# Optimization experiments

Hardware: AMD Instinct MI355X
Metric: run time of the kernel (lower is better)

The kernel has to match this reference:

```python
import jax, jax.numpy as jnp
import numpy as np

V_TH = 1.0          # HeavisideBoxcar firing threshold
SUBTHRESH = 0.5     # boxcar surrogate half-width (affects backward only)
INIT_TAU = 2.0      # membrane time constant; decay = sigmoid(init_tau)

N_IN, N_HIDDEN = 784, 1024
BATCH, STEPS = 128, 500


def setup_inputs() -> dict:
    key = jax.random.key(0)
    kx, kf, kr = jax.random.split(key, 3)
    x = jax.random.uniform(kx, (BATCH, STEPS, N_IN), dtype=jnp.float32)
    fc1 = 0.05 * jax.random.uniform(kf, (N_IN, N_HIDDEN), dtype=jnp.float32) / np.sqrt(N_IN)
    recurrent = 0.05 * jax.random.uniform(kr, (N_HIDDEN, N_HIDDEN), dtype=jnp.float32) / np.sqrt(N_HIDDEN)
    return {"x": x, "fc1": fc1, "recurrent": recurrent}


def reference(x, fc1, recurrent):
    # x: [B, T, n_in]; leaky-integrate-and-fire recurrent scan over T.
    B, T, _ = x.shape
    n_hidden = fc1.shape[1]
    n_slice = n_hidden // 10
    decay = jax.nn.sigmoid(jnp.asarray(INIT_TAU, dtype=x.dtype))

    def step(carry, x_t):
        mem, spk = carry                                   # [B, H] each
        cur = x_t @ fc1 + spk @ recurrent                  # input + recurrent current
        mem = mem * decay * (1.0 - spk) + cur              # leaky integrate with reset-by-spike
        spk = (mem >= V_TH).astype(mem.dtype)              # heaviside fire
        return (mem, spk), spk[:, :n_slice]

    init = (jnp.zeros((B, n_hidden), x.dtype), jnp.zeros((B, n_hidden), x.dtype))
    _, outs = jax.lax.scan(step, init, jnp.swapaxes(x, 0, 1))   # outs: [T, B, n_slice]
    return jnp.swapaxes(outs, 0, 1), T
```

## Files before the change

kernel.cpp:

```cpp
#include <hip/hip_runtime.h>
#include <stdint.h>

#define T_STEPS 500
#define NBATCH  128
#define NIN     784
#define KPAD    832
#define NH      1024
#define NSL     102
#define DECAY   0.8807970779778823f

typedef __attribute__((ext_vector_type(8))) short short8;
typedef __attribute__((ext_vector_type(4))) float f32x4;
typedef unsigned int u32;
typedef unsigned long long u64;

static __device__ __forceinline__ unsigned short f2bf(float f) {
  union { float f; u32 u; } v; v.f = f;
  u32 r = (v.u + 0x7FFFu + ((v.u >> 16) & 1u)) >> 16;
  return (unsigned short)r;
}
static __device__ __forceinline__ float uf(u32 u) {
  union { u32 u; float f; } v; v.u = u; return v.f;
}
static __device__ __forceinline__ u32 fu(float f) {
  union { float f; u32 u; } v; v.f = f; return v.u;
}
static __device__ __forceinline__ void gl16(const void* g, void* l) {
  __builtin_amdgcn_global_load_lds((const __attribute__((address_space(1))) u32*)g,
                                   (__attribute__((address_space(3))) u32*)l, 16, 0, 0);
}

__global__ __launch_bounds__(256) void prep_kernel(
    const float* __restrict__ fc1, unsigned short* __restrict__ fc1T,
    float* __restrict__ out_last) {
  __shared__ float tile[32][33];
  const int bx = blockIdx.x;
  const int kb = (bx % 26) * 32, nb = (bx / 26) * 32;
  const int tx = threadIdx.x & 31, ty = threadIdx.x >> 5;
#pragma unroll
  for (int i = 0; i < 4; ++i) {
    int k = kb + ty + i * 8, n = nb + tx;
    tile[ty + i * 8][tx] = (k < NIN) ? fc1[(size_t)k * NH + n] : 0.0f;
  }
  __syncthreads();
#pragma unroll
  for (int i = 0; i < 4; ++i) {
    int n = nb + ty + i * 8, k = kb + tx;
    fc1T[(size_t)n * KPAD + k] = f2bf(tile[tx][ty + i * 8]);
  }
  if (bx == 0 && threadIdx.x == 0) *out_last = 500.0f;
}

__global__ __launch_bounds__(256, 2) void gemm_kernel(
    const float* __restrict__ x, const unsigned short* __restrict__ fc1T,
    const float* __restrict__ wrec, float* __restrict__ colsum,
    unsigned short* __restrict__ curq) {
  if (blockIdx.y == 500) {
    const int h = blockIdx.x * 256 + threadIdx.x;
    float s0 = 0.f, s1 = 0.f, s2 = 0.f, s3 = 0.f,
          s4 = 0.f, s5 = 0.f, s6 = 0.f, s7 = 0.f;
    for (int j = 0; j < NH; j += 8) {
      s0 += wrec[(size_t)(j + 0) * NH + h];
      s1 += wrec[(size_t)(j + 1) * NH + h];
      s2 += wrec[(size_t)(j + 2) * NH + h];
      s3 += wrec[(size_t)(j + 3) * NH + h];
      s4 += wrec[(size_t)(j + 4) * NH + h];
      s5 += wrec[(size_t)(j + 5) * NH + h];
      s6 += wrec[(size_t)(j + 6) * NH + h];
      s7 += wrec[(size_t)(j + 7) * NH + h];
    }
    colsum[h] = ((s0 + s1) + (s2 + s3)) + ((s4 + s5) + (s6 + s7));
    return;
  }

  __shared__ __align__(16) float Af[128 * 64];
  __shared__ __align__(16) unsigned short Bs[256 * 64];

  const int tid = threadIdx.x;
  const int n0 = blockIdx.x * 256, m0 = blockIdx.y * 128;
  const int lane = tid & 63, wave = tid >> 6;
  const int wr = (wave >> 1) * 64, wc = (wave & 1) * 128;
  const int l16 = lane & 15, q = lane >> 4;

  const int a_r = lane >> 4;
  const int a_pc = lane & 15;
  const int b_r = lane >> 3;
  const int b_pc = lane & 7;

  f32x4 acc[4][8];
  const f32x4 z4 = {0.f, 0.f, 0.f, 0.f};
#pragma unroll
  for (int i = 0; i < 4; ++i)
#pragma unroll
    for (int j = 0; j < 8; ++j) acc[i][j] = z4;

  for (int k0 = 0; k0 < KPAD; k0 += 64) {
#pragma unroll
    for (int l = 0; l < 8; ++l) {
      const int rbase = wave * 32 + l * 4;
      const int row = rbase + a_r;
      const int g = a_pc ^ (row & 15);
      if (k0 + g * 4 < NIN)
        gl16(x + (size_t)(m0 + row) * NIN + k0 + g * 4, &Af[rbase * 64]);
    }
#pragma unroll
    for (int l = 0; l < 8; ++l) {
      const int rbase = wave * 64 + l * 8;
      const int row = rbase + b_r;
      const int g = b_pc ^ (row & 7);
      gl16(fc1T + (size_t)(n0 + row) * KPAD + k0 + g * 8, &Bs[rbase * 64]);
    }
    __syncthreads();

#pragma unroll
    for (int h = 0; h < 2; ++h) {
      short8 av[4], bv[8];
#pragma unroll
      for (int i = 0; i < 4; ++i) {
        const int r = wr + i * 16 + l16;
        const int g0 = h * 8 + q * 2;
        const float4 alo = *(const float4*)&Af[r * 64 + ((g0)     ^ (r & 15)) * 4];
        const float4 ahi = *(const float4*)&Af[r * 64 + ((g0 + 1) ^ (r & 15)) * 4];
        union { short8 s; u32 u[4]; } p;
        p.u[0] = __builtin_amdgcn_perm(fu(alo.y), fu(alo.x), 0x07060302u);
        p.u[1] = __builtin_amdgcn_perm(fu(alo.w), fu(alo.z), 0x07060302u);
        p.u[2] = __builtin_amdgcn_perm(fu(ahi.y), fu(ahi.x), 0x07060302u);
        p.u[3] = __builtin_amdgcn_perm(fu(ahi.w), fu(ahi.z), 0x07060302u);
        av[i] = p.s;
      }
#pragma unroll
      for (int j = 0; j < 8; ++j) {
        const int r = wc + j * 16 + l16;
        const int c = h * 4 + q;
        bv[j] = *(const short8*)&Bs[r * 64 + ((c ^ (r & 7))) * 8];
      }
#pragma unroll
      for (int i = 0; i < 4; ++i)
#pragma unroll
        for (int j = 0; j < 8; ++j)
          acc[i][j] = __builtin_amdgcn_mfma_f32_16x16x32_bf16(av[i], bv[j],
                                                              acc[i][j], 0, 0, 0);
    }
    __syncthreads();
  }

#pragma unroll
  for (int i = 0; i < 4; ++i)
#pragma unroll
    for (int j = 0; j < 8; ++j) {
      const int row = m0 + wr + i * 16 + q * 4;
      const int col = n0 + wc + j * 16 + l16;
#pragma unroll
      for (int rr = 0; rr < 4; ++rr)
        curq[(size_t)(row + rr) * NH + col] = f2bf(acc[i][j][rr]);
    }
}

template <int NP, int NL>
static __device__ __forceinline__ void scan_blk(
    const int tb, const size_t rowbase, const int h0, const unsigned lane,
    const unsigned short* __restrict__ curq, const float* __restrict__ wrec,
    const float* __restrict__ colsum, float* __restrict__ out,
    uint4 (&cur)[8][2], uint4 (&nxt)[8][2],
    float (&mem)[16], float (&rs)[16], float (&sp)[16],
    u32& spbits, u32& chgpack, u64& pend) {
#pragma unroll
  for (int u = 0; u < NL; ++u) {
    const uint4* p = (const uint4*)&curq[(rowbase + tb + 8 + u) * NH + h0];
    nxt[u][0] = p[0];
    nxt[u][1] = p[1];
  }
#pragma unroll
  for (int u = 0; u < NP; ++u) {
    const int t = tb + u;

    if (__builtin_expect(pend != 0ull, 0)) {
      if (__popcll(pend) >= 48) {
#pragma unroll
        for (int c = 0; c < 16; c += 4) {
          const float4 cs = *(const float4*)&colsum[h0 + c];
          rs[c] = cs.x; rs[c + 1] = cs.y; rs[c + 2] = cs.z; rs[c + 3] = cs.w;
        }
        const u32 myz = (~spbits) & 0xFFFFu;
        u64 zm = __ballot(myz != 0);
        while (zm) {
          const int l = __builtin_ctzll(zm); zm &= zm - 1;
          u32 zb = __shfl(myz, l, 64);
          while (zb) {
            const int c = __builtin_ctz(zb); zb &= zb - 1;
            const float* w = &wrec[(size_t)(l * 16 + c) * NH + h0];
#pragma unroll
            for (int qq = 0; qq < 4; ++qq) {
              const float4 wv = *(const float4*)(w + 4 * qq);
              rs[4 * qq] -= wv.x; rs[4 * qq + 1] -= wv.y;
              rs[4 * qq + 2] -= wv.z; rs[4 * qq + 3] -= wv.w;
            }
          }
        }
      } else {
        u64 dm = pend;
        while (dm) {
          const int l = __builtin_ctzll(dm); dm &= dm - 1;
          const u32 pk = __shfl(chgpack, l, 64);
          u32 cbits = pk >> 16;
          while (cbits) {
            const int c = __builtin_ctz(cbits); cbits &= cbits - 1;
            const float s = ((pk >> c) & 1u) ? 1.0f : -1.0f;
            const float* w = &wrec[(size_t)(l * 16 + c) * NH + h0];
#pragma unroll
            for (int qq = 0; qq < 4; ++qq) {
              const float4 wv = *(const float4*)(w + 4 * qq);
              rs[4 * qq]     = fmaf(s, wv.x, rs[4 * qq]);
              rs[4 * qq + 1] = fmaf(s, wv.y, rs[4 * qq + 1]);
              rs[4 * qq + 2] = fmaf(s, wv.z, rs[4 * qq + 2]);
              rs[4 * qq + 3] = fmaf(s, wv.w, rs[4 * qq + 3]);
            }
          }
        }
      }
      pend = 0;
    }

    const uint4 Aa = cur[u][0], Bb = cur[u][1];
    const u32 dw[8] = {Aa.x, Aa.y, Aa.z, Aa.w, Bb.x, Bb.y, Bb.z, Bb.w};
    float cin[16];
#pragma unroll
    for (int k = 0; k < 8; ++k) {
      cin[2 * k]     = uf(dw[k] << 16);
      cin[2 * k + 1] = uf(dw[k] & 0xFFFF0000u);
    }

    u32 newbits = 0;
    float ns[16];
#pragma unroll
    for (int c = 0; c < 16; ++c) {
      const float f = fmaf(-DECAY, sp[c], DECAY);
      mem[c] = fmaf(mem[c], f, cin[c] + rs[c]);
      const bool fire = mem[c] >= 1.0f;
      ns[c] = fire ? 1.0f : 0.0f;
      newbits |= fire ? (1u << c) : 0u;
    }

    if (lane < 7) {
      float2* o = (float2*)(out + (rowbase + t) * NSL + h0);
      const int n2 = (lane == 6) ? 3 : 8;
#pragma unroll
      for (int k = 0; k < 8; ++k)
        if (k < n2) o[k] = make_float2(ns[2 * k], ns[2 * k + 1]);
    }

    const u32 chg = spbits ^ newbits;
    pend = __ballot(chg != 0);
    chgpack = (chg << 16) | newbits;
    spbits = newbits;
#pragma unroll
    for (int c = 0; c < 16; ++c) sp[c] = ns[c];
  }
}

__global__ __launch_bounds__(64, 1) void scan_kernel(
    const unsigned short* __restrict__ curq, const float* __restrict__ wrec,
    const float* __restrict__ colsum, float* __restrict__ out) {
  const int b = blockIdx.x;
  const unsigned lane = threadIdx.x;
  const int h0 = (int)lane * 16;
  const size_t rowbase = (size_t)b * T_STEPS;

  float mem[16], rs[16], sp[16];
#pragma unroll
  for (int c = 0; c < 16; ++c) { mem[c] = 0.f; rs[c] = 0.f; sp[c] = 0.f; }
  u32 spbits = 0, chgpack = 0;
  u64 pend = 0;

  uint4 A[8][2], B[8][2];
#pragma unroll
  for (int u = 0; u < 8; ++u) {
    const uint4* p = (const uint4*)&curq[(rowbase + u) * NH + h0];
    A[u][0] = p[0];
    A[u][1] = p[1];
  }

  int tb = 0;
#pragma unroll 1
  for (int it = 0; it < 30; ++it) {
    scan_blk<8, 8>(tb, rowbase, h0, lane, curq, wrec, colsum, out,
                   A, B, mem, rs, sp, spbits, chgpack, pend);
    scan_blk<8, 8>(tb + 8, rowbase, h0, lane, curq, wrec, colsum, out,
                   B, A, mem, rs, sp, spbits, chgpack, pend);
    tb += 16;
  }
  scan_blk<8, 8>(480, rowbase, h0, lane, curq, wrec, colsum, out,
                 A, B, mem, rs, sp, spbits, chgpack, pend);
  scan_blk<8, 4>(488, rowbase, h0, lane, curq, wrec, colsum, out,
                 B, A, mem, rs, sp, spbits, chgpack, pend);
  scan_blk<4, 0>(496, rowbase, h0, lane, curq, wrec, colsum, out,
                 A, B, mem, rs, sp, spbits, chgpack, pend);
}

extern "C" void kernel_launch(void* const* d_in, const int* in_sizes, int n_in,
                              void* d_out, int out_size, void* d_ws, size_t ws_size,
                              hipStream_t stream) {
  const float* x    = (const float*)d_in[0];
  const float* fc1  = (const float*)d_in[1];
  const float* wrec = (const float*)d_in[2];
  float* out = (float*)d_out;

  unsigned short* fc1T = (unsigned short*)d_ws;
  float* colsum = (float*)((char*)d_ws + 1703936);
  unsigned short* curq = (unsigned short*)((char*)d_ws + 1708032);

  prep_kernel<<<dim3(26 * 32), 256, 0, stream>>>(fc1, fc1T, out + (out_size - 1));
  gemm_kernel<<<dim3(4, 501), 256, 0, stream>>>(x, fc1T, wrec, colsum, curq);
  scan_kernel<<<dim3(NBATCH), 64, 0, stream>>>(curq, wrec, colsum, out);
}
```

Before: 632.2 us.

## Shrink GEMM tile, convert A to bf16 at load, and restructure scan prefetch

The GEMM tile changes from 128x256 to 128x128, doubling the grid and raising launch bounds to 3 blocks per SM. The fp32 x tile is now converted to bf16 in registers before it is written to LDS, which halves A's shared-memory footprint, and the extra colsum blocks are told to exit early. The scan kernel replaces the 8-deep double-buffered block prefetch with a 4-deep rolling per-row prefetch written as macros. These changes aim for higher occupancy and lower LDS use in the GEMM and less register pressure in the scan. The cost is a shallower prefetch distance in the serial scan, and the A loads become synchronous register loads instead of direct-to-LDS loads.

```diff
diff --git a/kernel.cpp b/kernel.cpp
--- a/kernel.cpp
+++ b/kernel.cpp
@@ -51,11 +51,12 @@
   if (bx == 0 && threadIdx.x == 0) *out_last = 500.0f;
 }
 
-__global__ __launch_bounds__(256, 2) void gemm_kernel(
+__global__ __launch_bounds__(256, 3) void gemm_kernel(
     const float* __restrict__ x, const unsigned short* __restrict__ fc1T,
     const float* __restrict__ wrec, float* __restrict__ colsum,
     unsigned short* __restrict__ curq) {
   if (blockIdx.y == 500) {
+    if (blockIdx.x >= 4) return;
     const int h = blockIdx.x * 256 + threadIdx.x;
     float s0 = 0.f, s1 = 0.f, s2 = 0.f, s3 = 0.f,
           s4 = 0.f, s5 = 0.f, s6 = 0.f, s7 = 0.f;
@@ -73,71 +74,76 @@
     return;
   }
 
-  __shared__ __align__(16) float Af[128 * 64];
-  __shared__ __align__(16) unsigned short Bs[256 * 64];
+  __shared__ __align__(16) unsigned short Aq[128 * 64];
+  __shared__ __align__(16) unsigned short Bs[128 * 64];
 
   const int tid = threadIdx.x;
-  const int n0 = blockIdx.x * 256, m0 = blockIdx.y * 128;
+  const int n0 = blockIdx.x * 128, m0 = blockIdx.y * 128;
   const int lane = tid & 63, wave = tid >> 6;
-  const int wr = (wave >> 1) * 64, wc = (wave & 1) * 128;
+  const int wr = (wave >> 1) * 64, wc = (wave & 1) * 64;
   const int l16 = lane & 15, q = lane >> 4;
 
-  const int a_r = lane >> 4;
-  const int a_pc = lane & 15;
-  const int b_r = lane >> 3;
-  const int b_pc = lane & 7;
-
-  f32x4 acc[4][8];
+  const int ar = tid >> 3;
+  const int ac = tid & 7;
+
+  f32x4 acc[4][4];
   const f32x4 z4 = {0.f, 0.f, 0.f, 0.f};
 #pragma unroll
   for (int i = 0; i < 4; ++i)
 #pragma unroll
-    for (int j = 0; j < 8; ++j) acc[i][j] = z4;
+    for (int j = 0; j < 4; ++j) acc[i][j] = z4;
 
   for (int k0 = 0; k0 < KPAD; k0 += 64) {
-#pragma unroll
-    for (int l = 0; l < 8; ++l) {
-      const int rbase = wave * 32 + l * 4;
-      const int row = rbase + a_r;
-      const int g = a_pc ^ (row & 15);
-      if (k0 + g * 4 < NIN)
-        gl16(x + (size_t)(m0 + row) * NIN + k0 + g * 4, &Af[rbase * 64]);
-    }
-#pragma unroll
-    for (int l = 0; l < 8; ++l) {
-      const int rbase = wave * 64 + l * 8;
-      const int row = rbase + b_r;
-      const int g = b_pc ^ (row & 7);
+    float4 fa[4][2];
+    const bool aval = (k0 + ac * 8) < NIN;
+#pragma unroll
+    for (int i = 0; i < 4; ++i) {
+      if (aval) {
+        const float4* src =
+            (const float4*)(x + (size_t)(m0 + i * 32 + ar) * NIN + k0 + ac * 8);
+        fa[i][0] = src[0];
+        fa[i][1] = src[1];
+      } else {
+        fa[i][0] = make_float4(0.f, 0.f, 0.f, 0.f);
+        fa[i][1] = make_float4(0.f, 0.f, 0.f, 0.f);
+      }
+    }
+#pragma unroll
+    for (int l = 0; l < 4; ++l) {
+      const int rbase = wave * 32 + l * 8;
+      const int row = rbase + (lane >> 3);
+      const int g = (lane & 7) ^ (row & 7);
       gl16(fc1T + (size_t)(n0 + row) * KPAD + k0 + g * 8, &Bs[rbase * 64]);
     }
+#pragma unroll
+    for (int i = 0; i < 4; ++i) {
+      union { short8 s; u32 u[4]; } p;
+      p.u[0] = __builtin_amdgcn_perm(fu(fa[i][0].y), fu(fa[i][0].x), 0x07060302u);
+      p.u[1] = __builtin_amdgcn_perm(fu(fa[i][0].w), fu(fa[i][0].z), 0x07060302u);
+      p.u[2] = __builtin_amdgcn_perm(fu(fa[i][1].y), fu(fa[i][1].x), 0x07060302u);
+      p.u[3] = __builtin_amdgcn_perm(fu(fa[i][1].w), fu(fa[i][1].z), 0x07060302u);
+      const int row = i * 32 + ar;
+      *(short8*)&Aq[row * 64 + (ac ^ (row & 7)) * 8] = p.s;
+    }
     __syncthreads();
 
 #pragma unroll
     for (int h = 0; h < 2; ++h) {
-      short8 av[4], bv[8];
+      short8 av[4], bv[4];
 #pragma unroll
       for (int i = 0; i < 4; ++i) {
         const int r = wr + i * 16 + l16;
-        const int g0 = h * 8 + q * 2;
-        const float4 alo = *(const float4*)&Af[r * 64 + ((g0)     ^ (r & 15)) * 4];
-        const float4 ahi = *(const float4*)&Af[r * 64 + ((g0 + 1) ^ (r & 15)) * 4];
-        union { short8 s; u32 u[4]; } p;
-        p.u[0] = __builtin_amdgcn_perm(fu(alo.y), fu(alo.x), 0x07060302u);
-        p.u[1] = __builtin_amdgcn_perm(fu(alo.w), fu(alo.z), 0x07060302u);
-        p.u[2] = __builtin_amdgcn_perm(fu(ahi.y), fu(ahi.x), 0x07060302u);
-        p.u[3] = __builtin_amdgcn_perm(fu(ahi.w), fu(ahi.z), 0x07060302u);
-        av[i] = p.s;
+        av[i] = *(const short8*)&Aq[r * 64 + ((h * 4 + q) ^ (r & 7)) * 8];
       }
 #pragma unroll
-      for (int j = 0; j < 8; ++j) {
+      for (int j = 0; j < 4; ++j) {
         const int r = wc + j * 16 + l16;
-        const int c = h * 4 + q;
-        bv[j] = *(const short8*)&Bs[r * 64 + ((c ^ (r & 7))) * 8];
+        bv[j] = *(const short8*)&Bs[r * 64 + ((h * 4 + q) ^ (r & 7)) * 8];
       }
 #pragma unroll
       for (int i = 0; i < 4; ++i)
 #pragma unroll
-        for (int j = 0; j < 8; ++j)
+        for (int j = 0; j < 4; ++j)
           acc[i][j] = __builtin_amdgcn_mfma_f32_16x16x32_bf16(av[i], bv[j],
                                                               acc[i][j], 0, 0, 0);
     }
@@ -147,7 +153,7 @@
 #pragma unroll
   for (int i = 0; i < 4; ++i)
 #pragma unroll
-    for (int j = 0; j < 8; ++j) {
+    for (int j = 0; j < 4; ++j) {
       const int row = m0 + wr + i * 16 + q * 4;
       const int col = n0 + wc + j * 16 + l16;
 #pragma unroll
@@ -156,107 +162,86 @@
     }
 }
 
-template <int NP, int NL>
-static __device__ __forceinline__ void scan_blk(
-    const int tb, const size_t rowbase, const int h0, const unsigned lane,
-    const unsigned short* __restrict__ curq, const float* __restrict__ wrec,
-    const float* __restrict__ colsum, float* __restrict__ out,
-    uint4 (&cur)[8][2], uint4 (&nxt)[8][2],
-    float (&mem)[16], float (&rs)[16], float (&sp)[16],
-    u32& spbits, u32& chgpack, u64& pend) {
-#pragma unroll
-  for (int u = 0; u < NL; ++u) {
-    const uint4* p = (const uint4*)&curq[(rowbase + tb + 8 + u) * NH + h0];
-    nxt[u][0] = p[0];
-    nxt[u][1] = p[1];
-  }
-#pragma unroll
-  for (int u = 0; u < NP; ++u) {
-    const int t = tb + u;
-
-    if (__builtin_expect(pend != 0ull, 0)) {
-      if (__popcll(pend) >= 48) {
-#pragma unroll
-        for (int c = 0; c < 16; c += 4) {
-          const float4 cs = *(const float4*)&colsum[h0 + c];
-          rs[c] = cs.x; rs[c + 1] = cs.y; rs[c + 2] = cs.z; rs[c + 3] = cs.w;
-        }
-        const u32 myz = (~spbits) & 0xFFFFu;
-        u64 zm = __ballot(myz != 0);
-        while (zm) {
-          const int l = __builtin_ctzll(zm); zm &= zm - 1;
-          u32 zb = __shfl(myz, l, 64);
-          while (zb) {
-            const int c = __builtin_ctz(zb); zb &= zb - 1;
-            const float* w = &wrec[(size_t)(l * 16 + c) * NH + h0];
-#pragma unroll
-            for (int qq = 0; qq < 4; ++qq) {
-              const float4 wv = *(const float4*)(w + 4 * qq);
-              rs[4 * qq] -= wv.x; rs[4 * qq + 1] -= wv.y;
-              rs[4 * qq + 2] -= wv.z; rs[4 * qq + 3] -= wv.w;
-            }
-          }
-        }
-      } else {
-        u64 dm = pend;
-        while (dm) {
-          const int l = __builtin_ctzll(dm); dm &= dm - 1;
-          const u32 pk = __shfl(chgpack, l, 64);
-          u32 cbits = pk >> 16;
-          while (cbits) {
-            const int c = __builtin_ctz(cbits); cbits &= cbits - 1;
-            const float s = ((pk >> c) & 1u) ? 1.0f : -1.0f;
-            const float* w = &wrec[(size_t)(l * 16 + c) * NH + h0];
-#pragma unroll
-            for (int qq = 0; qq < 4; ++qq) {
-              const float4 wv = *(const float4*)(w + 4 * qq);
-              rs[4 * qq]     = fmaf(s, wv.x, rs[4 * qq]);
-              rs[4 * qq + 1] = fmaf(s, wv.y, rs[4 * qq + 1]);
-              rs[4 * qq + 2] = fmaf(s, wv.z, rs[4 * qq + 2]);
-              rs[4 * qq + 3] = fmaf(s, wv.w, rs[4 * qq + 3]);
-            }
-          }
-        }
-      }
-      pend = 0;
-    }
-
-    const uint4 Aa = cur[u][0], Bb = cur[u][1];
-    const u32 dw[8] = {Aa.x, Aa.y, Aa.z, Aa.w, Bb.x, Bb.y, Bb.z, Bb.w};
-    float cin[16];
-#pragma unroll
-    for (int k = 0; k < 8; ++k) {
-      cin[2 * k]     = uf(dw[k] << 16);
-      cin[2 * k + 1] = uf(dw[k] & 0xFFFF0000u);
-    }
-
-    u32 newbits = 0;
-    float ns[16];
-#pragma unroll
-    for (int c = 0; c < 16; ++c) {
-      const float f = fmaf(-DECAY, sp[c], DECAY);
-      mem[c] = fmaf(mem[c], f, cin[c] + rs[c]);
-      const bool fire = mem[c] >= 1.0f;
-      ns[c] = fire ? 1.0f : 0.0f;
-      newbits |= fire ? (1u << c) : 0u;
-    }
-
-    if (lane < 7) {
-      float2* o = (float2*)(out + (rowbase + t) * NSL + h0);
-      const int n2 = (lane == 6) ? 3 : 8;
-#pragma unroll
-      for (int k = 0; k < 8; ++k)
-        if (k < n2) o[k] = make_float2(ns[2 * k], ns[2 * k + 1]);
-    }
-
-    const u32 chg = spbits ^ newbits;
-    pend = __ballot(chg != 0);
-    chgpack = (chg << 16) | newbits;
-    spbits = newbits;
-#pragma unroll
-    for (int c = 0; c < 16; ++c) sp[c] = ns[c];
-  }
-}
+#define LOADROW(T, QA, QB)                                              \
+  {                                                                     \
+    const uint4* _p = (const uint4*)&curq[(rowbase + (T)) * NH + h0];   \
+    (QA) = _p[0];                                                       \
+    (QB) = _p[1];                                                       \
+  }
+
+#define STEP(T, QA, QB)                                                       \
+  {                                                                           \
+    if (__builtin_expect(pend != 0ull, 0)) {                                  \
+      if (__popcll(pend) >= 48) {        \
+        _Pragma("unroll") for (int c = 0; c < 16; c += 4) {                   \
+          const float4 cs = *(const float4*)&colsum[h0 + c];                  \
+          rs[c] = cs.x; rs[c + 1] = cs.y; rs[c + 2] = cs.z; rs[c + 3] = cs.w; \
+        }                                                                     \
+        const u32 myz = (~spbits) & 0xFFFFu;                                  \
+        u64 zm = __ballot(myz != 0);                                          \
+        while (zm) {                                                          \
+          const int l = __builtin_ctzll(zm); zm &= zm - 1;                    \
+          u32 zb = __shfl(myz, l, 64);                                        \
+          while (zb) {                                                        \
+            const int c = __builtin_ctz(zb); zb &= zb - 1;                    \
+            const float* w = &wrec[(size_t)(l * 16 + c) * NH + h0];           \
+            _Pragma("unroll") for (int qq = 0; qq < 4; ++qq) {                \
+              const float4 wv = *(const float4*)(w + 4 * qq);                 \
+              rs[4 * qq] -= wv.x; rs[4 * qq + 1] -= wv.y;                     \
+              rs[4 * qq + 2] -= wv.z; rs[4 * qq + 3] -= wv.w;                 \
+            }                                                                 \
+          }                                                                   \
+        }                                                                     \
+      } else {                                                                \
+        u64 dm = pend;                                                        \
+        while (dm) {                                                          \
+          const int l = __builtin_ctzll(dm); dm &= dm - 1;                    \
+          const u32 pk = __shfl(chgpack, l, 64);                              \
+          u32 cbits = pk >> 16;                                               \
+          while (cbits) {                                                     \
+            const int c = __builtin_ctz(cbits); cbits &= cbits - 1;           \
+            const float s = ((pk >> c) & 1u) ? 1.0f : -1.0f;                  \
+            const float* w = &wrec[(size_t)(l * 16 + c) * NH + h0];           \
+            _Pragma("unroll") for (int qq = 0; qq < 4; ++qq) {                \
+              const float4 wv = *(const float4*)(w + 4 * qq);                 \
+              rs[4 * qq]     = fmaf(s, wv.x, rs[4 * qq]);                     \
+              rs[4 * qq + 1] = fmaf(s, wv.y, rs[4 * qq + 1]);                 \
+              rs[4 * qq + 2] = fmaf(s, wv.z, rs[4 * qq + 2]);                 \
+              rs[4 * qq + 3] = fmaf(s, wv.w, rs[4 * qq + 3]);                 \
+            }                                                                 \
+          }                                                                   \
+        }                                                                     \
+      }                                                                       \
+      pend = 0;                                                               \
+    }                                                                         \
+    const u32 dw[8] = {(QA).x, (QA).y, (QA).z, (QA).w,                        \
+                       (QB).x, (QB).y, (QB).z, (QB).w};                       \
+    float cin[16];                                                            \
+    _Pragma("unroll") for (int k = 0; k < 8; ++k) {                           \
+      cin[2 * k]     = uf(dw[k] << 16);                                       \
+      cin[2 * k + 1] = uf(dw[k] & 0xFFFF0000u);                               \
+    }                                                                         \
+    u32 newbits = 0;                                                          \
+    float ns[16];                                                             \
+    _Pragma("unroll") for (int c = 0; c < 16; ++c) {                          \
+      const float f = fmaf(-DECAY, sp[c], DECAY);                             \
+      mem[c] = fmaf(mem[c], f, cin[c] + rs[c]);                               \
+      const bool fire = mem[c] >= 1.0f;                                       \
+      ns[c] = fire ? 1.0f : 0.0f;                                             \
+      newbits |= fire ? (1u << c) : 0u;                                       \
+    }                                                                         \
+    if (lane < 7) {                                                           \
+      float2* o = (float2*)(out + (rowbase + (T)) * NSL + h0);                \
+      const int n2 = (lane == 6) ? 3 : 8;                                     \
+      _Pragma("unroll") for (int k = 0; k < 8; ++k)                           \
+        if (k < n2) o[k] = make_float2(ns[2 * k], ns[2 * k + 1]);             \
+    }                                                                         \
+    const u32 chg = spbits ^ newbits;                                         \
+    pend = __ballot(chg != 0);                                                \
+    chgpack = (chg << 16) | newbits;                                          \
+    spbits = newbits;                                                         \
+    _Pragma("unroll") for (int c = 0; c < 16; ++c) sp[c] = ns[c];             \
+  }
 
 __global__ __launch_bounds__(64, 1) void scan_kernel(
     const unsigned short* __restrict__ curq, const float* __restrict__ wrec,
@@ -272,29 +257,27 @@
   u32 spbits = 0, chgpack = 0;
   u64 pend = 0;
 
-  uint4 A[8][2], B[8][2];
-#pragma unroll
-  for (int u = 0; u < 8; ++u) {
-    const uint4* p = (const uint4*)&curq[(rowbase + u) * NH + h0];
-    A[u][0] = p[0];
-    A[u][1] = p[1];
-  }
-
-  int tb = 0;
+  uint4 p0a, p0b, p1a, p1b, p2a, p2b, p3a, p3b;
+  LOADROW(0, p0a, p0b)
+  LOADROW(1, p1a, p1b)
+  LOADROW(2, p2a, p2b)
+  LOADROW(3, p3a, p3b)
+
 #pragma unroll 1
-  for (int it = 0; it < 30; ++it) {
-    scan_blk<8, 8>(tb, rowbase, h0, lane, curq, wrec, colsum, out,
-                   A, B, mem, rs, sp, spbits, chgpack, pend);
-    scan_blk<8, 8>(tb + 8, rowbase, h0, lane, curq, wrec, colsum, out,
-                   B, A, mem, rs, sp, spbits, chgpack, pend);
-    tb += 16;
-  }
-  scan_blk<8, 8>(480, rowbase, h0, lane, curq, wrec, colsum, out,
-                 A, B, mem, rs, sp, spbits, chgpack, pend);
-  scan_blk<8, 4>(488, rowbase, h0, lane, curq, wrec, colsum, out,
-                 B, A, mem, rs, sp, spbits, chgpack, pend);
-  scan_blk<4, 0>(496, rowbase, h0, lane, curq, wrec, colsum, out,
-                 A, B, mem, rs, sp, spbits, chgpack, pend);
+  for (int tb = 0; tb < T_STEPS - 4; tb += 4) {
+    STEP(tb + 0, p0a, p0b)
+    LOADROW(tb + 4, p0a, p0b)
+    STEP(tb + 1, p1a, p1b)
+    LOADROW(tb + 5, p1a, p1b)
+    STEP(tb + 2, p2a, p2b)
+    LOADROW(tb + 6, p2a, p2b)
+    STEP(tb + 3, p3a, p3b)
+    LOADROW(tb + 7, p3a, p3b)
+  }
+  STEP(T_STEPS - 4, p0a, p0b)
+  STEP(T_STEPS - 3, p1a, p1b)
+  STEP(T_STEPS - 2, p2a, p2b)
+  STEP(T_STEPS - 1, p3a, p3b)
 }
 
 extern "C" void kernel_launch(void* const* d_in, const int* in_sizes, int n_in,
@@ -310,6 +293,6 @@
   unsigned short* curq = (unsigned short*)((char*)d_ws + 1708032);
 
   prep_kernel<<<dim3(26 * 32), 256, 0, stream>>>(fc1, fc1T, out + (out_size - 1));
-  gemm_kernel<<<dim3(4, 501), 256, 0, stream>>>(x, fc1T, wrec, colsum, curq);
+  gemm_kernel<<<dim3(8, 501), 256, 0, stream>>>(x, fc1T, wrec, colsum, curq);
   scan_kernel<<<dim3(NBATCH), 64, 0, stream>>>(curq, wrec, colsum, out);
 }
```

Result: slower. 880.4 us (+39.3%).
